# Kernel optimization log

Hardware: AMD Instinct MI355X
Metric: run time of the kernel (lower is better)

## Reference

```python
import jax, jax.numpy as jnp
import numpy as np

NPOINT = 1024
RADIUS = 0.2
NSAMPLE = 32


def setup_inputs() -> dict:
    key = jax.random.key(0)
    ks = jax.random.split(key, 8)
    B, N, C = 8, 8192, 64
    xyz = jax.random.uniform(ks[0], (B, N, 3), dtype=jnp.float32)
    features = jax.random.normal(ks[1], (B, N, C), dtype=jnp.float32)
    c_in = C + 3  # QueryAndGroup concatenates relative xyz with features
    s = 0.05
    w1 = jax.random.normal(ks[2], (c_in, 64), dtype=jnp.float32) * s
    b1 = jnp.zeros((64,), jnp.float32)
    w2 = jax.random.normal(ks[3], (64, 64), dtype=jnp.float32) * s
    b2 = jnp.zeros((64,), jnp.float32)
    w3 = jax.random.normal(ks[4], (64, 128), dtype=jnp.float32) * s
    b3 = jnp.zeros((128,), jnp.float32)
    return {"xyz": xyz, "features": features, "w1": w1, "b1": b1,
            "w2": w2, "b2": b2, "w3": w3, "b3": b3}


def farthest_point_sample(xyz, npoint):
    # xyz: (B, N, 3) -> (B, npoint) int32 indices
    B, N, _ = xyz.shape

    def step(carry, _):
        dist, far = carry
        centroid = jnp.take_along_axis(xyz, far[:, None, None], axis=1)  # (B,1,3)
        d = jnp.sum((xyz - centroid) ** 2, axis=-1)  # (B,N)
        dist = jnp.minimum(dist, d)
        nxt = jnp.argmax(dist, axis=-1).astype(jnp.int32)
        return (dist, nxt), far

    init = (jnp.full((B, N), 1e10, jnp.float32), jnp.zeros((B,), jnp.int32))
    _, idxs = jax.lax.scan(step, init, None, length=npoint)
    return idxs.T  # (B, npoint)


def ball_query(radius, nsample, xyz, new_xyz):
    # returns (B, S, nsample) int32 neighbor indices into N
    sq = jnp.sum((new_xyz[:, :, None, :] - xyz[:, None, :, :]) ** 2, axis=-1)  # (B,S,N)
    B, S, N = sq.shape
    idx = jnp.broadcast_to(jnp.arange(N, dtype=jnp.int32), (B, S, N))
    idx = jnp.where(sq > radius * radius, N, idx)
    idx = jnp.sort(idx, axis=-1)[:, :, :nsample]
    first = idx[:, :, :1]
    idx = jnp.where(idx == N, first, idx)  # pad with first valid index
    return idx


_gather = jax.vmap(lambda pts, idx: pts[idx])  # per-batch fancy gather


def reference(xyz, features, w1, b1, w2, b2, w3, b3):
    fps_idx = farthest_point_sample(xyz, NPOINT)
    new_xyz = _gather(xyz, fps_idx)  # (B, S, 3)
    nbr_idx = ball_query(RADIUS, NSAMPLE, xyz, new_xyz)  # (B, S, K)
    g_xyz = _gather(xyz, nbr_idx) - new_xyz[:, :, None, :]  # (B,S,K,3) relative coords
    g_feat = _gather(features, nbr_idx)  # (B, S, K, C)
    x = jnp.concatenate([g_xyz, g_feat], axis=-1)  # (B, S, K, C+3)
    # shared pointwise MLP (Conv2d 1x1 + ReLU)
    x = jax.nn.relu(x @ w1 + b1)
    x = jax.nn.relu(x @ w2 + b2)
    x = jax.nn.relu(x @ w3 + b3)
    new_features = jnp.max(x, axis=2)  # max-pool over neighbors -> (B, S, 128)
    return new_xyz, jnp.transpose(new_features, (0, 2, 1))  # (B,S,3), (B,128,S)
```

## Files before the change

### kernel.cpp

```cpp
#include <hip/hip_runtime.h>
#include <stdint.h>

#define N_PTS 8192
#define B_SZ 8
#define NPOINT_ 1024
#define NSAMPLE_ 32
#define NPROD 8
#define NCONS 240
#define CWAVES (NCONS * 8)

typedef float __attribute__((ext_vector_type(2))) f32x2;

template <int CTRL>
__device__ __forceinline__ float dpp_maxf(float v) {
    int o = __builtin_amdgcn_update_dpp(__float_as_int(v), __float_as_int(v),
                                        CTRL, 0xf, 0xf, false);
    return fmaxf(v, __int_as_float(o));
}
template <int CTRL>
__device__ __forceinline__ int dpp_mini(int v) {
    int o = __builtin_amdgcn_update_dpp(v, v, CTRL, 0xf, 0xf, false);
    return (o < v) ? o : v;
}

__device__ __forceinline__ float ld_coh(const float* p) {
    return __int_as_float(__hip_atomic_load((int*)p, __ATOMIC_RELAXED,
                                            __HIP_MEMORY_SCOPE_AGENT));
}
__device__ __forceinline__ void st_coh(float* p, float v) {
    __hip_atomic_store((int*)p, __float_as_int(v), __ATOMIC_RELAXED,
                       __HIP_MEMORY_SCOPE_AGENT);
}

#define SM_SPTS 0
#define SM_CVAL 131072
#define SM_CIDX 131136
#define SM_W1 0
#define SM_W2 17920
#define SM_W3 34816
#define SM_B1 68608
#define SM_B2 68864
#define SM_B3 69120
#define SM_XB 69632
#define SM_HB 104448
#define SM_NIDX 139264
#define SM_TOTAL 140288

#define W1S 70
#define W2S 66
#define W3S 66

__global__ __launch_bounds__(512, 2) void fused_kernel(
    const float* __restrict__ xyz, const float* __restrict__ feat,
    const float* __restrict__ w1, const float* __restrict__ b1,
    const float* __restrict__ w2, const float* __restrict__ b2,
    const float* __restrict__ w3, const float* __restrict__ b3,
    float* __restrict__ new_xyz, float* __restrict__ out,
    int* __restrict__ prog) {
    __shared__ __align__(16) char smem[SM_TOTAL];
    const int t = threadIdx.x;
    const int wave = t >> 6, lane = t & 63;

    if (blockIdx.x < NPROD) {
        float4* spts = (float4*)smem;
        float* cval = (float*)(smem + SM_CVAL);
        int* cidx = (int*)(smem + SM_CIDX);
        const int b = blockIdx.x;
        const float* bx = xyz + (size_t)b * N_PTS * 3;
        int* pp = prog + b * 64;

        f32x2 px[8], py[8], pz[8], dst[8];
#pragma unroll
        for (int jj = 0; jj < 8; ++jj) {
            int p0 = t + 512 * (2 * jj);
            int p1 = t + 512 * (2 * jj + 1);
            float x0 = bx[3 * p0 + 0], y0 = bx[3 * p0 + 1], z0 = bx[3 * p0 + 2];
            float x1 = bx[3 * p1 + 0], y1 = bx[3 * p1 + 1], z1 = bx[3 * p1 + 2];
            spts[p0] = make_float4(x0, y0, z0, 0.0f);
            spts[p1] = make_float4(x1, y1, z1, 0.0f);
            px[jj] = f32x2{x0, x1};
            py[jj] = f32x2{y0, y1};
            pz[jj] = f32x2{z0, z1};
            dst[jj] = f32x2{1e10f, 1e10f};
        }
        __syncthreads();

        float cx = bx[0], cy = bx[1], cz = bx[2];
        int hold = 0;

        for (int it = 1; it < NPOINT_; ++it) {
            f32x2 cx2 = f32x2{cx, cx}, cy2 = f32x2{cy, cy}, cz2 = f32x2{cz, cz};
            {
#pragma clang fp contract(off)
#pragma unroll
                for (int jj = 0; jj < 8; ++jj) {
                    f32x2 dx = px[jj] - cx2;
                    f32x2 dy = py[jj] - cy2;
                    f32x2 dz = pz[jj] - cz2;
                    f32x2 d = (dx * dx + dy * dy) + dz * dz;
                    dst[jj] = __builtin_elementwise_min(dst[jj], d);
                }
            }
            f32x2 m01 = __builtin_elementwise_max(dst[0], dst[1]);
            f32x2 m23 = __builtin_elementwise_max(dst[2], dst[3]);
            f32x2 m45 = __builtin_elementwise_max(dst[4], dst[5]);
            f32x2 m67 = __builtin_elementwise_max(dst[6], dst[7]);
            f32x2 m03 = __builtin_elementwise_max(m01, m23);
            f32x2 m47 = __builtin_elementwise_max(m45, m67);
            f32x2 mm = __builtin_elementwise_max(m03, m47);
            float bv = fmaxf(mm.x, mm.y);
            int lj = 0;
#pragma unroll
            for (int jj = 7; jj >= 0; --jj) {
                lj = (dst[jj].y == bv) ? 2 * jj + 1 : lj;
                lj = (dst[jj].x == bv) ? 2 * jj : lj;
            }
            int idx = (lj << 9) + t;

            float mv = bv;
            mv = dpp_maxf<0x111>(mv);
            mv = dpp_maxf<0x112>(mv);
            mv = dpp_maxf<0x114>(mv);
            mv = dpp_maxf<0x118>(mv);
            mv = dpp_maxf<0x142>(mv);
            mv = dpp_maxf<0x143>(mv);
            float wmax = __int_as_float(
                __builtin_amdgcn_readlane(__float_as_int(mv), 63));
            int ic = (bv == wmax) ? idx : 0x7FFFFFFF;
            ic = dpp_mini<0x111>(ic);
            ic = dpp_mini<0x112>(ic);
            ic = dpp_mini<0x114>(ic);
            ic = dpp_mini<0x118>(ic);
            ic = dpp_mini<0x142>(ic);
            ic = dpp_mini<0x143>(ic);

            const int buf = it & 1;
            if (lane == 63) {
                cval[buf * 8 + wave] = wmax;
                cidx[buf * 8 + wave] = ic;
            }
            __syncthreads();

            if ((it & 63) == 0 && t == 0) {
                __hip_atomic_store(pp, it, __ATOMIC_RELAXED,
                                   __HIP_MEMORY_SCOPE_AGENT);
            }

            float cv = cval[buf * 8 + (lane & 7)];
            int ci = cidx[buf * 8 + (lane & 7)];
            float gm = cv;
            gm = dpp_maxf<0x111>(gm);
            gm = dpp_maxf<0x112>(gm);
            gm = dpp_maxf<0x114>(gm);
            float gmax =
                __int_as_float(__builtin_amdgcn_readlane(__float_as_int(gm), 7));
            int ic2 = (cv == gmax) ? ci : 0x7FFFFFFF;
            ic2 = dpp_mini<0x111>(ic2);
            ic2 = dpp_mini<0x112>(ic2);
            ic2 = dpp_mini<0x114>(ic2);
            int wi = __builtin_amdgcn_readlane(ic2, 7);

            hold = (lane == (it & 63)) ? wi : hold;

            float4 sp = spts[wi];
            cx = sp.x;
            cy = sp.y;
            cz = sp.z;

            if ((it & 63) == 63 && wave == 0) {
                float4 me = spts[hold];
                int s0 = b * NPOINT_ + (it - 63) + lane;
                st_coh(&new_xyz[s0 * 3 + 0], me.x);
                st_coh(&new_xyz[s0 * 3 + 1], me.y);
                st_coh(&new_xyz[s0 * 3 + 2], me.z);
            }
        }
        __syncthreads();
        if (t == 0) {
            __hip_atomic_store(pp, NPOINT_, __ATOMIC_RELAXED,
                               __HIP_MEMORY_SCOPE_AGENT);
        }
    } else {
        float* lw1T = (float*)(smem + SM_W1);
        float* lw2T = (float*)(smem + SM_W2);
        float* lw3T = (float*)(smem + SM_W3);
        float* lb1 = (float*)(smem + SM_B1);
        float* lb2 = (float*)(smem + SM_B2);
        float* lb3 = (float*)(smem + SM_B3);

        for (int i = t; i < 67 * 64; i += 512) {
            int k = i >> 6, c = i & 63;
            lw1T[c * W1S + k] = w1[i];
        }
        if (t < 64) lw1T[t * W1S + 67] = 0.0f;
        for (int i = t; i < 64 * 64; i += 512) {
            int k = i >> 6, c = i & 63;
            lw2T[c * W2S + k] = w2[i];
        }
        for (int i = t; i < 64 * 128; i += 512) {
            int k = i >> 7, c = i & 127;
            lw3T[c * W3S + k] = w3[i];
        }
        if (t < 64) {
            lb1[t] = b1[t];
            lb2[t] = b2[t];
        }
        if (t < 128) lb3[t] = b3[t];
        __syncthreads();

        float* xw = (float*)(smem + SM_XB) + wave * (16 * 68);
        float* hw = (float*)(smem + SM_HB) + wave * (16 * 68);
        int* nw = (int*)(smem + SM_NIDX) + wave * 32;
        const float* wc1 = lw1T + lane * W1S;
        const float* wc2 = lw2T + lane * W2S;
        const float* wca = lw3T + lane * W3S;
        const float* wcb = lw3T + (lane + 64) * W3S;

        const int widx = (blockIdx.x - NPROD) * 8 + wave;
        for (int cc = widx; cc < B_SZ * NPOINT_; cc += CWAVES) {
            const int s = cc >> 3, b = cc & 7;
            const int g = (b << 10) + s;
            int* pp = prog + b * 64;

            int pv = __hip_atomic_load(pp, __ATOMIC_RELAXED,
                                       __HIP_MEMORY_SCOPE_AGENT);
            while (pv <= s) {
                if (s - pv >= 64)
                    __builtin_amdgcn_s_sleep(64);
                else
                    __builtin_amdgcn_s_sleep(16);
                pv = __hip_atomic_load(pp, __ATOMIC_RELAXED,
                                       __HIP_MEMORY_SCOPE_AGENT);
            }
            __builtin_amdgcn_fence(__ATOMIC_ACQUIRE, "agent");
            const float cx = ld_coh(&new_xyz[g * 3 + 0]);
            const float cy = ld_coh(&new_xyz[g * 3 + 1]);
            const float cz = ld_coh(&new_xyz[g * 3 + 2]);

            const float* bx = xyz + (size_t)b * N_PTS * 3;
            const float r2 = 0.04f;
            int taken = 0, firstIdx = -1;
            for (int ch = 0; ch < N_PTS / 64 && taken < NSAMPLE_; ++ch) {
                int p = ch * 64 + lane;
                float dxq = __fsub_rn(bx[3 * p + 0], cx);
                float dyq = __fsub_rn(bx[3 * p + 1], cy);
                float dzq = __fsub_rn(bx[3 * p + 2], cz);
                float sq = __fadd_rn(
                    __fadd_rn(__fmul_rn(dxq, dxq), __fmul_rn(dyq, dyq)),
                    __fmul_rn(dzq, dzq));
                bool pred = !(sq > r2);
                unsigned long long mask = __ballot(pred);
                if (mask) {
                    int cnt = __popcll(mask);
                    if (firstIdx < 0) firstIdx = ch * 64 + (__ffsll(mask) - 1);
                    if (pred) {
                        int pos =
                            taken + __popcll(mask & ((1ull << lane) - 1ull));
                        if (pos < NSAMPLE_) nw[pos] = p;
                    }
                    taken += cnt;
                }
            }
            if (lane >= taken && lane < NSAMPLE_) nw[lane] = firstIdx;
            asm volatile("s_waitcnt lgkmcnt(0)" ::: "memory");

            float mo0 = 0.0f, mo1 = 0.0f;
            for (int half = 0; half < 2; ++half) {
                int iis[16];
#pragma unroll
                for (int r = 0; r < 16; ++r) iis[r] = nw[half * 16 + r];
#pragma unroll
                for (int r = 0; r < 16; ++r) {
                    xw[r * 68 + 3 + lane] =
                        feat[((size_t)b * N_PTS + iis[r]) * 64 + lane];
                    if (lane < 3) {
                        float pv2 = xyz[((size_t)b * N_PTS + iis[r]) * 3 + lane];
                        float cv = (lane == 0) ? cx : ((lane == 1) ? cy : cz);
                        xw[r * 68 + lane] = pv2 - cv;
                    }
                    if (lane == 0) xw[r * 68 + 67] = 0.0f;
                }
                f32x2 acc2[16];
                {
                    float bias = lb1[lane];
#pragma unroll
                    for (int r = 0; r < 16; ++r) acc2[r] = f32x2{bias, 0.0f};
                    for (int kk = 0; kk < 68; kk += 4) {
                        f32x2 wA = *(const f32x2*)(wc1 + kk);
                        f32x2 wB = *(const f32x2*)(wc1 + kk + 2);
#pragma unroll
                        for (int r = 0; r < 16; ++r) {
                            float4 xv = *(const float4*)&xw[r * 68 + kk];
                            f32x2 xa = f32x2{xv.x, xv.y};
                            f32x2 xc = f32x2{xv.z, xv.w};
                            acc2[r] = xa * wA + acc2[r];
                            acc2[r] = xc * wB + acc2[r];
                        }
                    }
#pragma unroll
                    for (int r = 0; r < 16; ++r)
                        hw[r * 68 + lane] = fmaxf(acc2[r].x + acc2[r].y, 0.0f);
                }
                {
                    float bias = lb2[lane];
#pragma unroll
                    for (int r = 0; r < 16; ++r) acc2[r] = f32x2{bias, 0.0f};
                    for (int kk = 0; kk < 64; kk += 4) {
                        f32x2 wA = *(const f32x2*)(wc2 + kk);
                        f32x2 wB = *(const f32x2*)(wc2 + kk + 2);
#pragma unroll
                        for (int r = 0; r < 16; ++r) {
                            float4 hv = *(const float4*)&hw[r * 68 + kk];
                            f32x2 xa = f32x2{hv.x, hv.y};
                            f32x2 xc = f32x2{hv.z, hv.w};
                            acc2[r] = xa * wA + acc2[r];
                            acc2[r] = xc * wB + acc2[r];
                        }
                    }
#pragma unroll
                    for (int r = 0; r < 16; ++r)
                        xw[r * 68 + lane] = fmaxf(acc2[r].x + acc2[r].y, 0.0f);
                }
                {
                    f32x2 a2[16], c2[16];
                    float bb0 = lb3[lane], bb1 = lb3[lane + 64];
#pragma unroll
                    for (int r = 0; r < 16; ++r) {
                        a2[r] = f32x2{bb0, 0.0f};
                        c2[r] = f32x2{bb1, 0.0f};
                    }
                    for (int kk = 0; kk < 64; kk += 4) {
                        f32x2 wA0 = *(const f32x2*)(wca + kk);
                        f32x2 wB0 = *(const f32x2*)(wca + kk + 2);
                        f32x2 wA1 = *(const f32x2*)(wcb + kk);
                        f32x2 wB1 = *(const f32x2*)(wcb + kk + 2);
#pragma unroll
                        for (int r = 0; r < 16; ++r) {
                            float4 hv = *(const float4*)&xw[r * 68 + kk];
                            f32x2 xa = f32x2{hv.x, hv.y};
                            f32x2 xc = f32x2{hv.z, hv.w};
                            a2[r] = xa * wA0 + a2[r];
                            a2[r] = xc * wB0 + a2[r];
                            c2[r] = xa * wA1 + c2[r];
                            c2[r] = xc * wB1 + c2[r];
                        }
                    }
#pragma unroll
                    for (int r = 0; r < 16; ++r) {
                        mo0 = fmaxf(mo0, fmaxf(a2[r].x + a2[r].y, 0.0f));
                        mo1 = fmaxf(mo1, fmaxf(c2[r].x + c2[r].y, 0.0f));
                    }
                }
            }
            out[((size_t)b * 128 + lane) * 1024 + s] = mo0;
            out[((size_t)b * 128 + lane + 64) * 1024 + s] = mo1;
        }
    }
}

extern "C" void kernel_launch(void* const* d_in, const int* in_sizes, int n_in,
                              void* d_out, int out_size, void* d_ws,
                              size_t ws_size, hipStream_t stream) {
    const float* xyz = (const float*)d_in[0];
    const float* feat = (const float*)d_in[1];
    const float* w1 = (const float*)d_in[2];
    const float* b1 = (const float*)d_in[3];
    const float* w2 = (const float*)d_in[4];
    const float* b2 = (const float*)d_in[5];
    const float* w3 = (const float*)d_in[6];
    const float* b3 = (const float*)d_in[7];

    float* out_xyz = (float*)d_out;
    float* out_feat = (float*)d_out + B_SZ * NPOINT_ * 3;
    int* prog = (int*)d_ws;

    hipMemsetAsync(d_ws, 0, NPROD * 64 * sizeof(int), stream);
    fused_kernel<<<NPROD + NCONS, 512, 0, stream>>>(
        xyz, feat, w1, b1, w2, b2, w3, b3, out_xyz, out_feat, prog);
}
```

Measured before the change: 1.023 ms.

## Publish FPS indices instead of coordinates and shrink consumer grid

```diff
diff --git a/kernel.cpp b/kernel.cpp
--- a/kernel.cpp
+++ b/kernel.cpp
@@ -6,7 +6,7 @@
 #define NPOINT_ 1024
 #define NSAMPLE_ 32
 #define NPROD 8
-#define NCONS 240
+#define NCONS 64
 #define CWAVES (NCONS * 8)
 
 typedef float __attribute__((ext_vector_type(2))) f32x2;
@@ -21,15 +21,6 @@
 __device__ __forceinline__ int dpp_mini(int v) {
     int o = __builtin_amdgcn_update_dpp(v, v, CTRL, 0xf, 0xf, false);
     return (o < v) ? o : v;
-}
-
-__device__ __forceinline__ float ld_coh(const float* p) {
-    return __int_as_float(__hip_atomic_load((int*)p, __ATOMIC_RELAXED,
-                                            __HIP_MEMORY_SCOPE_AGENT));
-}
-__device__ __forceinline__ void st_coh(float* p, float v) {
-    __hip_atomic_store((int*)p, __float_as_int(v), __ATOMIC_RELAXED,
-                       __HIP_MEMORY_SCOPE_AGENT);
 }
 
 #define SM_SPTS 0
@@ -50,16 +41,20 @@
 #define W2S 66
 #define W3S 66
 
+#define WS_ILIST_OFF 512
+
 __global__ __launch_bounds__(512, 2) void fused_kernel(
     const float* __restrict__ xyz, const float* __restrict__ feat,
     const float* __restrict__ w1, const float* __restrict__ b1,
     const float* __restrict__ w2, const float* __restrict__ b2,
     const float* __restrict__ w3, const float* __restrict__ b3,
     float* __restrict__ new_xyz, float* __restrict__ out,
-    int* __restrict__ prog) {
+    int* __restrict__ ws) {
     __shared__ __align__(16) char smem[SM_TOTAL];
     const int t = threadIdx.x;
     const int wave = t >> 6, lane = t & 63;
+    int* prog = ws;
+    int* ilist = ws + WS_ILIST_OFF;
 
     if (blockIdx.x < NPROD) {
         float4* spts = (float4*)smem;
@@ -168,11 +163,8 @@
             cz = sp.z;
 
             if ((it & 63) == 63 && wave == 0) {
-                float4 me = spts[hold];
-                int s0 = b * NPOINT_ + (it - 63) + lane;
-                st_coh(&new_xyz[s0 * 3 + 0], me.x);
-                st_coh(&new_xyz[s0 * 3 + 1], me.y);
-                st_coh(&new_xyz[s0 * 3 + 2], me.z);
+                __hip_atomic_store(&ilist[(b << 10) + (it - 63) + lane], hold,
+                                   __ATOMIC_RELAXED, __HIP_MEMORY_SCOPE_AGENT);
             }
         }
         __syncthreads();
@@ -225,17 +217,25 @@
             int pv = __hip_atomic_load(pp, __ATOMIC_RELAXED,
                                        __HIP_MEMORY_SCOPE_AGENT);
             while (pv <= s) {
-                if (s - pv >= 64)
+                int d = s - pv;
+                if (d >= 128)
+                    __builtin_amdgcn_s_sleep(127);
+                else if (d >= 32)
                     __builtin_amdgcn_s_sleep(64);
                 else
-                    __builtin_amdgcn_s_sleep(16);
+                    __builtin_amdgcn_s_sleep(8);
                 pv = __hip_atomic_load(pp, __ATOMIC_RELAXED,
                                        __HIP_MEMORY_SCOPE_AGENT);
             }
             __builtin_amdgcn_fence(__ATOMIC_ACQUIRE, "agent");
-            const float cx = ld_coh(&new_xyz[g * 3 + 0]);
-            const float cy = ld_coh(&new_xyz[g * 3 + 1]);
-            const float cz = ld_coh(&new_xyz[g * 3 + 2]);
+            const int cix = __hip_atomic_load(&ilist[g], __ATOMIC_RELAXED,
+                                              __HIP_MEMORY_SCOPE_AGENT);
+            const float* cp = xyz + ((size_t)b * N_PTS + cix) * 3;
+            const float cx = cp[0];
+            const float cy = cp[1];
+            const float cz = cp[2];
+            if (lane < 3)
+                new_xyz[g * 3 + lane] = (lane == 0) ? cx : ((lane == 1) ? cy : cz);
 
             const float* bx = xyz + (size_t)b * N_PTS * 3;
             const float r2 = 0.04f;
@@ -372,9 +372,9 @@
 
     float* out_xyz = (float*)d_out;
     float* out_feat = (float*)d_out + B_SZ * NPOINT_ * 3;
-    int* prog = (int*)d_ws;
-
-    hipMemsetAsync(d_ws, 0, NPROD * 64 * sizeof(int), stream);
+    int* ws = (int*)d_ws;
+
+    hipMemsetAsync(d_ws, 0, WS_ILIST_OFF * sizeof(int), stream);
     fused_kernel<<<NPROD + NCONS, 512, 0, stream>>>(
-        xyz, feat, w1, b1, w2, b2, w3, b3, out_xyz, out_feat, prog);
+        xyz, feat, w1, b1, w2, b2, w3, b3, out_xyz, out_feat, ws);
 }
```

Measured after the change: 1.023 ms. About the same (+0.0%).
